# Performance work log

Measured on AMD Instinct MI355X. Metric: run time of the kernel, lower is better.

## Reference

```python
import jax, jax.numpy as jnp
import numpy as np

VOCAB = 32000
D = 512
OUT = 1000
L = 2
H = 8
HD = D // H
MAX_SEQ = 128
ALPHA = 0.5
B, S = 8, 128


def _layernorm(h, g, b, eps=1e-5):
    mu = jnp.mean(h, axis=-1, keepdims=True)
    var = jnp.mean(jnp.square(h - mu), axis=-1, keepdims=True)
    return (h - mu) * jax.lax.rsqrt(var + eps) * g + b


def setup_inputs() -> dict:
    key = jax.random.key(0)
    ks = jax.random.split(key, 20)
    sd = 1.0 / np.sqrt(D)
    inp = {
        "x": jax.random.randint(ks[0], (B, S), 0, VOCAB),
        "steps": 20,
        "tok_emb": jax.random.normal(ks[1], (VOCAB, D), jnp.float32) * 0.02,
        "pos_emb": jax.random.normal(ks[2], (MAX_SEQ, D), jnp.float32) * 0.02,
        # per-layer stacked weights (linear as x @ W + b)
        "Wq": jax.random.normal(ks[3], (L, D, D), jnp.float32) * sd,
        "bq": jnp.zeros((L, D), jnp.float32),
        "Wk": jax.random.normal(ks[4], (L, D, D), jnp.float32) * sd,
        "bk": jnp.zeros((L, D), jnp.float32),
        "Wv": jax.random.normal(ks[5], (L, D, D), jnp.float32) * sd,
        "bv": jnp.zeros((L, D), jnp.float32),
        "Wo": jax.random.normal(ks[6], (L, D, D), jnp.float32) * sd,
        "bo": jnp.zeros((L, D), jnp.float32),
        "W1": jax.random.normal(ks[7], (L, D, 2 * D), jnp.float32) * sd,
        "b1": jnp.zeros((L, 2 * D), jnp.float32),
        "W2": jax.random.normal(ks[8], (L, 2 * D, D), jnp.float32) * (1.0 / np.sqrt(2 * D)),
        "b2": jnp.zeros((L, D), jnp.float32),
        "ln1_g": jnp.ones((L, D), jnp.float32),
        "ln1_b": jnp.zeros((L, D), jnp.float32),
        "ln2_g": jnp.ones((L, D), jnp.float32),
        "ln2_b": jnp.zeros((L, D), jnp.float32),
        "head_w": jax.random.normal(ks[9], (D, OUT), jnp.float32) * sd,
        "head_b": jnp.zeros((OUT,), jnp.float32),
    }
    return inp


def _forward(x, steps, tok_emb, pos_emb, Wq, bq, Wk, bk, Wv, bv, Wo, bo,
             W1, b1, W2, b2, ln1_g, ln1_b, ln2_g, ln2_b, head_w, head_b):
    b, s = x.shape
    x_emb = tok_emb[x] + pos_emb[jnp.arange(s)][None, :, :]  # [B,S,D]
    scale = 1.0 / np.sqrt(HD)

    def step(h, _):
        for i in range(L):
            hn = _layernorm(h, ln1_g[i], ln1_b[i])
            q = (hn @ Wq[i] + bq[i]).reshape(b, s, H, HD)
            k = (hn @ Wk[i] + bk[i]).reshape(b, s, H, HD)
            v = (hn @ Wv[i] + bv[i]).reshape(b, s, H, HD)
            scores = jnp.einsum('bqhd,bkhd->bhqk', q, k) * scale
            attn = jax.nn.softmax(scores, axis=-1)
            o = jnp.einsum('bhqk,bkhd->bqhd', attn, v).reshape(b, s, D)
            h = h + (o @ Wo[i] + bo[i])
            hn2 = _layernorm(h, ln2_g[i], ln2_b[i])
            ffn = jax.nn.relu(hn2 @ W1[i] + b1[i]) @ W2[i] + b2[i]
            h_target = h + ffn + x_emb
            h = h + ALPHA * (jnp.tanh(h_target) - h)  # lerp(h, tanh(t), alpha)
        return h, None

    h0 = jnp.zeros_like(x_emb)
    h, _ = jax.lax.scan(step, h0, None, length=steps)
    return h.mean(axis=1) @ head_w + head_b  # [B, OUT]


def reference(x, steps, tok_emb, pos_emb, Wq, bq, Wk, bk, Wv, bv, Wo, bo,
              W1, b1, W2, b2, ln1_g, ln1_b, ln2_g, ln2_b, head_w, head_b):
    return _forward(x, steps, tok_emb, pos_emb, Wq, bq, Wk, bk, Wv, bv, Wo, bo,
                    W1, b1, W2, b2, ln1_g, ln1_b, ln2_g, ln2_b, head_w, head_b)
```

## Files before the change

### kernel.cpp

```cpp
#include <hip/hip_runtime.h>
#include <hip/hip_bf16.h>
#include <math.h>

#define NTOK 1024
#define DM   512
#define NB   256

typedef unsigned short u16;
typedef __attribute__((ext_vector_type(8))) short short8;
typedef __attribute__((ext_vector_type(4))) float f32x4;
typedef __attribute__((ext_vector_type(2))) float f32x2;
typedef __attribute__((address_space(1))) const void* as1cv;
typedef __attribute__((address_space(3))) void* as3v;

#define VM12 0x0F7C
#define VM16 0x4F70
#define VM8  0x0F78
#define VM0  0x0F70

__device__ inline u16 f2bf(float f) {
  __hip_bfloat16 h = __float2bfloat16(f);
  return *reinterpret_cast<u16*>(&h);
}
__device__ inline float bf2f(u16 b) {
  union { unsigned u; float f; } x; x.u = (unsigned)b << 16; return x.f;
}
__device__ inline void split8(const float* v, short8& hi, short8& lo) {
#pragma unroll
  for (int j = 0; j < 8; j++) {
    u16 h = f2bf(v[j]);
    hi[j] = (short)h;
    lo[j] = (short)f2bf(v[j] - bf2f(h));
  }
}
__device__ __forceinline__ f32x4 MFMA(short8 a, short8 b, f32x4 c) {
  return __builtin_amdgcn_mfma_f32_16x16x32_bf16(a, b, c, 0, 0, 0);
}
__device__ __forceinline__ void atomAddF(float* p, float v) {
  __hip_atomic_fetch_add(p, v, __ATOMIC_RELAXED, __HIP_MEMORY_SCOPE_AGENT);
}

__device__ __forceinline__ f32x2 ldg_cs2(const float* p) {
  f32x2 r;
  asm volatile("global_load_dwordx2 %0, %1, off sc0 sc1" : "=v"(r) : "v"(p) : "memory");
  return r;
}
__device__ __forceinline__ void vmwait0() {
  asm volatile("s_waitcnt vmcnt(0)" ::: "memory");
  __builtin_amdgcn_sched_barrier(0);
}

enum { EP_RESID = 1, EP_TANHLERP = 3 };

struct KArgs {
  const int* x;
  const float* tok; const float* pos;
  const float* W[6];
  const float* bias6[6];
  const float* ln1g; const float* ln1b; const float* ln2g; const float* ln2b;
  const float* hw; const float* hb;
  float* out;
  float* xe; float* h;
  u16* obh; u16* obl;
  u16* ffh; u16* ffl;
  u16* vT;
  float* hm;
  u16* WTh[6]; u16* WTl[6];
  float* ln1sum; float* ln2sum;
  unsigned* bar;
};

#define SMEM_BYTES 49152

__device__ __forceinline__ void bar_arrive(unsigned* ctr, int tid) {
  __syncthreads();
  if (tid == 0)
    __hip_atomic_fetch_add(ctr, 1u, __ATOMIC_RELEASE, __HIP_MEMORY_SCOPE_AGENT);
}
__device__ __forceinline__ void bar_wait(unsigned* ctr, unsigned target, int tid) {
  if (tid == 0) {
    while (__hip_atomic_load(ctr, __ATOMIC_RELAXED, __HIP_MEMORY_SCOPE_AGENT) < target)
      __builtin_amdgcn_s_sleep(2);
    __builtin_amdgcn_fence(__ATOMIC_ACQUIRE, "agent");
  }
  __syncthreads();
}
__device__ __forceinline__ void bar_arrive_fast(unsigned* myslot, unsigned ph, int tid) {
  asm volatile("s_waitcnt vmcnt(0) lgkmcnt(0)" ::: "memory");
  __syncthreads();
  if (tid == 0)
    __hip_atomic_store(myslot, ph, __ATOMIC_RELAXED, __HIP_MEMORY_SCOPE_AGENT);
}
__device__ __forceinline__ void bar_wait_fast(unsigned* slotbase, unsigned ph, int tid) {
  if (tid < 32) {
    while (__hip_atomic_load(slotbase + tid * 16, __ATOMIC_RELAXED,
                             __HIP_MEMORY_SCOPE_AGENT) < ph)
      __builtin_amdgcn_s_sleep(1);
  }
  __syncthreads();
  asm volatile("buffer_inv sc0" ::: "memory");
  asm volatile("s_waitcnt vmcnt(0)" ::: "memory");
}
__global__ void bar_init(unsigned* bar) {
  for (int i = threadIdx.x; i < 8192; i += 256) bar[i] = 0u;
}

__device__ __forceinline__ void dmaW64(const u16* gbase, int K, int k0, u16* lds, int tid) {
  const int wave = tid >> 6, lane = tid & 63;
#pragma unroll
  for (int i = 0; i < 2; i++) {
    const int lc = wave * 128 + i * 64 + lane;
    const int n = lc >> 3, sl = lc & 7;
    const int c = sl ^ (n & 7);
    const u16* g = gbase + (size_t)n * K + k0 + c * 8;
    u16* dst = lds + (size_t)(wave * 128 + i * 64) * 8;
    __builtin_amdgcn_global_load_lds((as1cv)(const void*)g, (as3v)(void*)dst, 16, 0, 0);
  }
}
__device__ __forceinline__ int boff64(int n, int cp) { return n * 64 + ((cp ^ (n & 7)) << 3); }

__device__ __forceinline__ void dmaW32(const u16* gbase, int K, int k0, u16* lds, int tid) {
  const int wave = tid >> 6, lane = tid & 63;
  const int lc = wave * 64 + lane;
  const int p = lc >> 3, s3 = lc & 7;
  const int c3 = s3 ^ (p & 7);
  const int n = p * 2 + (c3 >> 2);
  const int c = c3 & 3;
  const u16* g = gbase + (size_t)n * K + k0 + c * 8;
  u16* dst = lds + (size_t)(wave * 64) * 8;
  __builtin_amdgcn_global_load_lds((as1cv)(const void*)g, (as3v)(void*)dst, 16, 0, 0);
}
__device__ __forceinline__ int boff32(int n, int cq) {
  const int c3 = ((n & 1) << 2) | cq;
  return ((n >> 1) << 6) + ((c3 ^ ((n >> 1) & 7)) << 3);
}

__device__ __forceinline__ void pfBD2(const u16* bh0, const u16* bl0, int K, char* sm, int tid) {
  dmaW64(bh0, K, 0,  (u16*)sm, tid);
  dmaW64(bl0, K, 0,  (u16*)sm + 4096, tid);
  dmaW64(bh0, K, 64, (u16*)(sm + 16384), tid);
  dmaW64(bl0, K, 64, (u16*)(sm + 16384) + 4096, tid);
}
__device__ __forceinline__ void pfA(const KArgs& a, int l, int head, char* sm, int tid) {
  const size_t o = (size_t)l * 512 * 512 + (size_t)head * 64 * 512;
  const u16* wz[6] = { a.WTh[0] + o, a.WTl[0] + o, a.WTh[1] + o,
                       a.WTl[1] + o, a.WTh[2] + o, a.WTl[2] + o };
#pragma unroll
  for (int z = 0; z < 6; z++) dmaW32(wz[z], 512, 0, (u16*)sm + z * 2048, tid);
}

__device__ void phaseA(const KArgs& a, int l, int head, int grp, const float* ln1,
                       const float* hR, u16* obh_g, u16* obl_g, char* sm, int tid)
{
  const int wave = tid >> 6, lane = tid & 63;
  const int q = lane >> 4, r16 = lane & 15;
  const int wm = (wave >> 1) * 32, wn = (wave & 1) * 32;
  const size_t wOff = (size_t)l * 512 * 512;
  const size_t hOff = (size_t)head * 64 * 512;

  const float* lg = a.ln1g + l * 512;
  const float* lb = a.ln1b + l * 512;
  const u16* wz[6] = { a.WTh[0] + wOff + hOff, a.WTl[0] + wOff + hOff,
                       a.WTh[1] + wOff + hOff, a.WTl[1] + wOff + hOff,
                       a.WTh[2] + wOff + hOff, a.WTl[2] + wOff + hOff };
  u16* vT = a.vT + (size_t)(grp * 8 + head) * 64 * 128;
  u16* buf[2] = { (u16*)sm, (u16*)sm + 12288 };

  int RB[4];
#pragma unroll
  for (int fi = 0; fi < 4; fi++) RB[fi] = (fi >> 1) * 64 + wm + (fi & 1) * 16;

  f32x2 st4[4];
#pragma unroll
  for (int fi = 0; fi < 4; fi++) st4[fi] = ldg_cs2(ln1 + (RB[fi] + r16) * 2);
  vmwait0();
  float mu[4], iv[4];
#pragma unroll
  for (int fi = 0; fi < 4; fi++) {
    const float m = st4[fi].x * (1.0f / 512.0f);
    mu[fi] = m;
    iv[fi] = rsqrtf(st4[fi].y * (1.0f / 512.0f) - m * m + 1e-5f);
  }

  f32x4 aq[4][2] = {}, ak[4][2] = {}, av[4][2] = {};

  float4 rA[4][2], rB4[4][2], rg[2], rb[2], rg2[2], rb2[2];
#pragma unroll
  for (int fi = 0; fi < 4; fi++) {
    const float* hp = hR + (size_t)(RB[fi] + r16) * DM + q * 8;
    rA[fi][0] = *(const float4*)hp; rA[fi][1] = *(const float4*)(hp + 4);
  }
  rg[0] = *(const float4*)&lg[q * 8]; rg[1] = *(const float4*)&lg[q * 8 + 4];
  rb[0] = *(const float4*)&lb[q * 8]; rb[1] = *(const float4*)&lb[q * 8 + 4];

  for (int ks = 0; ks < 16; ks++) {
    if (ks + 1 < 16) {
      const int kb = (ks + 1) * 32 + q * 8;
#pragma unroll
      for (int fi = 0; fi < 4; fi++) {
        const float* hp = hR + (size_t)(RB[fi] + r16) * DM + kb;
        rB4[fi][0] = *(const float4*)hp; rB4[fi][1] = *(const float4*)(hp + 4);
      }
      rg2[0] = *(const float4*)&lg[kb]; rg2[1] = *(const float4*)&lg[kb + 4];
      rb2[0] = *(const float4*)&lb[kb]; rb2[1] = *(const float4*)&lb[kb + 4];
      __builtin_amdgcn_s_waitcnt(VM12);
    } else {
      __builtin_amdgcn_s_waitcnt(VM0);
    }
    __builtin_amdgcn_s_barrier();
    if (ks + 1 < 16) {
      u16* nb = buf[(ks + 1) & 1];
#pragma unroll
      for (int z2 = 0; z2 < 6; z2++) dmaW32(wz[z2], 512, (ks + 1) * 32, nb + z2 * 2048, tid);
    }
    const u16* cb = buf[ks & 1];
    short8 ah[4], al[4];
#pragma unroll
    for (int fi = 0; fi < 4; fi++) {
      float v[8] = {
        (rA[fi][0].x - mu[fi]) * iv[fi] * rg[0].x + rb[0].x,
        (rA[fi][0].y - mu[fi]) * iv[fi] * rg[0].y + rb[0].y,
        (rA[fi][0].z - mu[fi]) * iv[fi] * rg[0].z + rb[0].z,
        (rA[fi][0].w - mu[fi]) * iv[fi] * rg[0].w + rb[0].w,
        (rA[fi][1].x - mu[fi]) * iv[fi] * rg[1].x + rb[1].x,
        (rA[fi][1].y - mu[fi]) * iv[fi] * rg[1].y + rb[1].y,
        (rA[fi][1].z - mu[fi]) * iv[fi] * rg[1].z + rb[1].z,
        (rA[fi][1].w - mu[fi]) * iv[fi] * rg[1].w + rb[1].w };
      split8(v, ah[fi], al[fi]);
    }
#pragma unroll
    for (int z = 0; z < 3; z++) {
      f32x4 (*ac)[2] = (z == 0) ? aq : ((z == 1) ? ak : av);
#pragma unroll
      for (int fj = 0; fj < 2; fj++) {
        const int n = wn + fj * 16 + r16;
        const int off = boff32(n, q);
        short8 bh = *(const short8*)&cb[(z * 2) * 2048 + off];
        short8 bl = *(const short8*)&cb[(z * 2 + 1) * 2048 + off];
#pragma unroll
        for (int fi = 0; fi < 4; fi++) {
          ac[fi][fj] = MFMA(ah[fi], bh, ac[fi][fj]);
          ac[fi][fj] = MFMA(ah[fi], bl, ac[fi][fj]);
          ac[fi][fj] = MFMA(al[fi], bh, ac[fi][fj]);
        }
      }
    }
#pragma unroll
    for (int fi = 0; fi < 4; fi++) { rA[fi][0] = rB4[fi][0]; rA[fi][1] = rB4[fi][1]; }
    rg[0] = rg2[0]; rg[1] = rg2[1]; rb[0] = rb2[0]; rb[1] = rb2[1];
  }
  __syncthreads();

  u16 (*Qb)[66] = (u16(*)[66])sm;
  u16 (*Kb)[66] = (u16(*)[66])(sm + 16896);
  {
    const float* bq = a.bias6[0] + l * 512 + head * 64;
    const float* bk = a.bias6[1] + l * 512 + head * 64;
    const float* bv = a.bias6[2] + l * 512 + head * 64;
#pragma unroll
    for (int fi = 0; fi < 4; fi++) {
#pragma unroll
      for (int fj = 0; fj < 2; fj++) {
        const int col = wn + fj * 16 + r16;
        const int row0 = RB[fi] + q * 4;
        const float bqv = bq[col], bkv = bk[col], bvv = bv[col];
#pragma unroll
        for (int i = 0; i < 4; i++) {
          Qb[row0 + i][col] = f2bf(aq[fi][fj][i] + bqv);
          Kb[row0 + i][col] = f2bf(ak[fi][fj][i] + bkv);
          vT[(size_t)col * 128 + row0 + i] = f2bf(av[fi][fj][i] + bvv);
        }
      }
    }
  }
  __syncthreads();

  const int m0 = wave * 32;
  f32x4 sc[2][8] = {};
#pragma unroll
  for (int kk = 0; kk < 2; kk++) {
    short8 aQ[2];
#pragma unroll
    for (int fi = 0; fi < 2; fi++)
      aQ[fi] = *(const short8*)&Qb[m0 + fi * 16 + r16][kk * 32 + q * 8];
#pragma unroll
    for (int nt = 0; nt < 8; nt++) {
      short8 bK = *(const short8*)&Kb[nt * 16 + r16][kk * 32 + q * 8];
#pragma unroll
      for (int fi = 0; fi < 2; fi++) sc[fi][nt] = MFMA(aQ[fi], bK, sc[fi][nt]);
    }
  }
  __syncthreads();

#pragma unroll
  for (int fi = 0; fi < 2; fi++) {
#pragma unroll
    for (int i = 0; i < 4; i++) {
      float mrow = -1e30f;
#pragma unroll
      for (int nt = 0; nt < 8; nt++) {
        float v = sc[fi][nt][i] * 0.125f; sc[fi][nt][i] = v; mrow = fmaxf(mrow, v);
      }
#pragma unroll
      for (int o = 1; o < 16; o <<= 1) mrow = fmaxf(mrow, __shfl_xor(mrow, o, 64));
      float lsum = 0.f;
#pragma unroll
      for (int nt = 0; nt < 8; nt++) {
        float p = __expf(sc[fi][nt][i] - mrow); sc[fi][nt][i] = p; lsum += p;
      }
#pragma unroll
      for (int o = 1; o < 16; o <<= 1) lsum += __shfl_xor(lsum, o, 64);
      const float inv = 1.0f / lsum;
#pragma unroll
      for (int nt = 0; nt < 8; nt++) sc[fi][nt][i] *= inv;
    }
  }
  u16 (*Pb)[132] = (u16(*)[132])sm;
#pragma unroll
  for (int fi = 0; fi < 2; fi++)
#pragma unroll
    for (int nt = 0; nt < 8; nt++)
#pragma unroll
      for (int i = 0; i < 4; i++)
        Pb[m0 + fi * 16 + q * 4 + i][nt * 16 + r16] = f2bf(sc[fi][nt][i]);
  __syncthreads();

  f32x4 oa[2][4] = {};
#pragma unroll
  for (int kt = 0; kt < 4; kt++) {
    short8 aP[2];
#pragma unroll
    for (int fi = 0; fi < 2; fi++)
      aP[fi] = *(const short8*)&Pb[m0 + fi * 16 + r16][kt * 32 + q * 8];
#pragma unroll
    for (int nt = 0; nt < 4; nt++) {
      short8 bV = *(const short8*)(vT + (size_t)(nt * 16 + r16) * 128 + kt * 32 + q * 8);
#pragma unroll
      for (int fi = 0; fi < 2; fi++) oa[fi][nt] = MFMA(aP[fi], bV, oa[fi][nt]);
    }
  }
#pragma unroll
  for (int fi = 0; fi < 2; fi++)
#pragma unroll
    for (int nt = 0; nt < 4; nt++)
#pragma unroll
      for (int i = 0; i < 4; i++) {
        const int row = m0 + fi * 16 + q * 4 + i;
        const int col = head * 64 + nt * 16 + r16;
        float v = oa[fi][nt][i];
        u16 hv = f2bf(v);
        obh_g[(size_t)row * DM + col] = hv;
        obl_g[(size_t)row * DM + col] = f2bf(v - bf2f(hv));
      }
}

template<int EP>
__device__ void tileBD(const u16* Ahi, const u16* Alo, int K,
                       const u16* Whi, const u16* Wlo, const float* bias,
                       int bm, int bn, float* hIO, const float* Xx,
                       float* lnacc, char* sm, int tid)
{
  const int wave = tid >> 6, lane = tid & 63;
  const int q = lane >> 4, r16 = lane & 15;
  const int wm = (wave >> 1) * 16, wn = (wave & 1) * 32;
  const u16* bh0 = Whi + (size_t)bn * K;
  const u16* bl0 = Wlo + (size_t)bn * K;
  f32x4 acc[2] = {};
  const int nk = K >> 6;

  short8 cah[2], cal[2], nh[2], nl[2];
#pragma unroll
  for (int kk = 0; kk < 2; kk++) {
    const size_t ao = (size_t)(bm + wm + r16) * K + kk * 32 + q * 8;
    cah[kk] = *(const short8*)(Ahi + ao);
    cal[kk] = *(const short8*)(Alo + ao);
  }

  for (int ks = 0; ks < nk; ks++) {
    if (ks + 1 < nk) {
#pragma unroll
      for (int kk = 0; kk < 2; kk++) {
        const size_t ao = (size_t)(bm + wm + r16) * K + (ks + 1) * 64 + kk * 32 + q * 8;
        nh[kk] = *(const short8*)(Ahi + ao);
        nl[kk] = *(const short8*)(Alo + ao);
      }
      __builtin_amdgcn_s_waitcnt(VM8);
    } else {
      __builtin_amdgcn_s_waitcnt(VM0);
    }
    __builtin_amdgcn_s_barrier();
    if (ks + 2 < nk) {
      u16* slot = (u16*)(sm + ((ks + 2) % 3) * 16384);
      dmaW64(bh0, K, (ks + 2) * 64, slot, tid);
      dmaW64(bl0, K, (ks + 2) * 64, slot + 4096, tid);
    }
    const u16* Bsh = (const u16*)(sm + (ks % 3) * 16384);
    const u16* Bsl = Bsh + 4096;
#pragma unroll
    for (int kk = 0; kk < 2; kk++) {
#pragma unroll
      for (int fj = 0; fj < 2; fj++) {
        const int n = wn + fj * 16 + r16;
        const int off = boff64(n, kk * 4 + q);
        short8 bh = *(const short8*)&Bsh[off];
        short8 bl = *(const short8*)&Bsl[off];
        acc[fj] = MFMA(cah[kk], bh, acc[fj]);
        acc[fj] = MFMA(cah[kk], bl, acc[fj]);
        acc[fj] = MFMA(cal[kk], bh, acc[fj]);
      }
    }
#pragma unroll
    for (int kk = 0; kk < 2; kk++) { cah[kk] = nh[kk]; cal[kk] = nl[kk]; }
  }

  float outv[2][4];
#pragma unroll
  for (int fj = 0; fj < 2; fj++) {
    const int col = bn + wn + fj * 16 + r16;
    const float bvv = bias[col];
    const int row0 = bm + wm + q * 4;
#pragma unroll
    for (int i = 0; i < 4; i++) {
      const size_t off = (size_t)(row0 + i) * DM + col;
      if (EP == EP_RESID) {
        float hv = hIO[off] + acc[fj][i] + bvv;
        hIO[off] = hv; outv[fj][i] = hv;
      } else {
        float hv = hIO[off];
        float hn = 0.5f * hv + 0.5f * tanhf(hv + acc[fj][i] + bvv + Xx[off]);
        hIO[off] = hn; outv[fj][i] = hn;
      }
    }
  }
#pragma unroll
  for (int i = 0; i < 4; i++) {
    float a0 = outv[0][i], a1 = outv[1][i];
    float s1 = a0 + a1, s2 = a0 * a0 + a1 * a1;
#pragma unroll
    for (int o = 1; o < 16; o <<= 1) { s1 += __shfl_xor(s1, o, 64); s2 += __shfl_xor(s2, o, 64); }
    if (r16 == 0) {
      const int row = bm + wm + q * 4 + i;
      atomAddF(&lnacc[row * 2], s1);
      atomAddF(&lnacc[row * 2 + 1], s2);
    }
  }
}

__device__ void tileC2(const KArgs& a, int l, const float* h_g, const float* lnsrc,
                       u16* ffh_g, u16* ffl_g, int bm, int bn0, char* sm, int tid)
{
  const int wave = tid >> 6, lane = tid & 63;
  const int q = lane >> 4, r16 = lane & 15;
  const int wm = (wave >> 1) * 16, wn = (wave & 1) * 32;
  const size_t fOff = (size_t)l * 512 * 1024;
  const float* lg = a.ln2g + l * 512;
  const float* lb = a.ln2b + l * 512;

  f32x2 stl = ldg_cs2(lnsrc + (bm + wm + r16) * 2);
  vmwait0();
  const float mu = stl.x * (1.0f / 512.0f);
  const float iv = rsqrtf(stl.y * (1.0f / 512.0f) - mu * mu + 1e-5f);

  const u16* whB[2] = { a.WTh[4] + fOff + (size_t)bn0 * 512,
                        a.WTh[4] + fOff + (size_t)(bn0 + 512) * 512 };
  const u16* wlB[2] = { a.WTl[4] + fOff + (size_t)bn0 * 512,
                        a.WTl[4] + fOff + (size_t)(bn0 + 512) * 512 };
  const float* b1 = a.bias6[4] + l * 1024;
  f32x4 acc[2] = {};

  float4 rA[2][2], rB4[2][2], rg[2][2], rb[2][2], rg2[2][2], rb2[2][2];
#pragma unroll
  for (int kk = 0; kk < 2; kk++) {
    const int kb = kk * 32 + q * 8;
    const float* hp = h_g + (size_t)(bm + wm + r16) * DM + kb;
    rA[kk][0] = *(const float4*)hp; rA[kk][1] = *(const float4*)(hp + 4);
    rg[kk][0] = *(const float4*)&lg[kb]; rg[kk][1] = *(const float4*)&lg[kb + 4];
    rb[kk][0] = *(const float4*)&lb[kb]; rb[kk][1] = *(const float4*)&lb[kb + 4];
  }

  for (int s = 0; s < 16; s++) {
    if (s + 1 < 16) {
      const int kb1 = ((s + 1) & 7) * 64;
#pragma unroll
      for (int kk = 0; kk < 2; kk++) {
        const int kb = kb1 + kk * 32 + q * 8;
        const float* hp = h_g + (size_t)(bm + wm + r16) * DM + kb;
        rB4[kk][0] = *(const float4*)hp; rB4[kk][1] = *(const float4*)(hp + 4);
        rg2[kk][0] = *(const float4*)&lg[kb]; rg2[kk][1] = *(const float4*)&lg[kb + 4];
        rb2[kk][0] = *(const float4*)&lb[kb]; rb2[kk][1] = *(const float4*)&lb[kb + 4];
      }
      __builtin_amdgcn_s_waitcnt(VM16);
    } else {
      __builtin_amdgcn_s_waitcnt(VM0);
    }
    __builtin_amdgcn_s_barrier();
    if (s + 2 < 16) {
      const int t2 = (s + 2) >> 3, k2 = ((s + 2) & 7) * 64;
      u16* slot = (u16*)(sm + ((s + 2) % 3) * 16384);
      dmaW64(whB[t2], 512, k2, slot, tid);
      dmaW64(wlB[t2], 512, k2, slot + 4096, tid);
    }
    const u16* Bsh = (const u16*)(sm + (s % 3) * 16384);
    const u16* Bsl = Bsh + 4096;
#pragma unroll
    for (int kk = 0; kk < 2; kk++) {
      short8 ah, al;
      {
        float v[8] = {
          (rA[kk][0].x - mu) * iv * rg[kk][0].x + rb[kk][0].x,
          (rA[kk][0].y - mu) * iv * rg[kk][0].y + rb[kk][0].y,
          (rA[kk][0].z - mu) * iv * rg[kk][0].z + rb[kk][0].z,
          (rA[kk][0].w - mu) * iv * rg[kk][0].w + rb[kk][0].w,
          (rA[kk][1].x - mu) * iv * rg[kk][1].x + rb[kk][1].x,
          (rA[kk][1].y - mu) * iv * rg[kk][1].y + rb[kk][1].y,
          (rA[kk][1].z - mu) * iv * rg[kk][1].z + rb[kk][1].z,
          (rA[kk][1].w - mu) * iv * rg[kk][1].w + rb[kk][1].w };
        split8(v, ah, al);
      }
#pragma unroll
      for (int fj = 0; fj < 2; fj++) {
        const int n = wn + fj * 16 + r16;
        const int off = boff64(n, kk * 4 + q);
        short8 bh = *(const short8*)&Bsh[off];
        short8 bl = *(const short8*)&Bsl[off];
        acc[fj] = MFMA(ah, bh, acc[fj]);
        acc[fj] = MFMA(ah, bl, acc[fj]);
        acc[fj] = MFMA(al, bh, acc[fj]);
      }
    }
    if ((s & 7) == 7) {
      const int t = s >> 3;
#pragma unroll
      for (int fj = 0; fj < 2; fj++) {
        const int col = bn0 + t * 512 + wn + fj * 16 + r16;
        const float bvv = b1[col];
        const int row0 = bm + wm + q * 4;
#pragma unroll
        for (int i = 0; i < 4; i++) {
          const size_t off = (size_t)(row0 + i) * 1024 + col;
          float r = fmaxf(acc[fj][i] + bvv, 0.f);
          u16 hv = f2bf(r);
          ffh_g[off] = hv; ffl_g[off] = f2bf(r - bf2f(hv));
        }
        acc[fj] = (f32x4){0.f, 0.f, 0.f, 0.f};
      }
    }
#pragma unroll
    for (int kk = 0; kk < 2; kk++) {
      rA[kk][0] = rB4[kk][0]; rA[kk][1] = rB4[kk][1];
      rg[kk][0] = rg2[kk][0]; rg[kk][1] = rg2[kk][1];
      rb[kk][0] = rb2[kk][0]; rb[kk][1] = rb2[kk][1];
    }
  }
}

__global__ __launch_bounds__(256, 1) void persist(KArgs a)
{
  __shared__ __align__(16) char smem[SMEM_BYTES];
  const int tid = threadIdx.x;
  const int bid = blockIdx.x;

  unsigned myxcd;
  asm volatile("s_getreg_b32 %0, hwreg(HW_REG_XCC_ID)" : "=s"(myxcd));
  myxcd &= 15u;
  if (tid == 0) a.bar[512 + bid] = myxcd;

  {
    float (*tile)[33] = (float (*)[33])smem;
    const int tx = tid & 31, ty = tid >> 5;
    for (int t = bid; t < 4096; t += NB) {
      int tensor, z, k0, n0, K, N;
      if (t < 2048)      { tensor = t >> 9;  int rem = t & 511;  z = rem >> 8; int r2 = rem & 255;
                           K = 512;  N = 512;  k0 = (r2 >> 4) << 5; n0 = (r2 & 15) << 5; }
      else if (t < 3072) { tensor = 4;       int rem = t - 2048; z = rem >> 9; int r2 = rem & 511;
                           K = 512;  N = 1024; k0 = (r2 >> 5) << 5; n0 = (r2 & 31) << 5; }
      else               { tensor = 5;       int rem = t - 3072; z = rem >> 9; int r2 = rem & 511;
                           K = 1024; N = 512;  k0 = (r2 >> 4) << 5; n0 = (r2 & 15) << 5; }
      const float* src = a.W[tensor]   + (size_t)z * K * N;
      u16* dhi         = a.WTh[tensor] + (size_t)z * K * N;
      u16* dlo         = a.WTl[tensor] + (size_t)z * K * N;
      __syncthreads();
#pragma unroll
      for (int r = 0; r < 4; r++) {
        int k = ty + r * 8;
        tile[k][tx] = src[(size_t)(k0 + k) * N + n0 + tx];
      }
      __syncthreads();
#pragma unroll
      for (int r = 0; r < 4; r++) {
        int n = ty + r * 8;
        float w = tile[tx][n];
        u16 hi = f2bf(w);
        dhi[(size_t)(n0 + n) * K + k0 + tx] = hi;
        dlo[(size_t)(n0 + n) * K + k0 + tx] = f2bf(w - bf2f(hi));
      }
    }
    for (int idx = bid * 256 + tid; idx < NTOK * DM; idx += NB * 256) {
      int t = idx >> 9, d = idx & 511, ss = t & 127;
      a.xe[idx] = a.tok[(size_t)a.x[t] * DM + d] + a.pos[ss * DM + d];
      a.h[idx] = 0.0f;
    }
    const int nstat = (41 + 40) * 8 * 256;
    for (int idx = bid * 256 + tid; idx < nstat; idx += NB * 256)
      a.ln1sum[idx] = 0.0f;
  }
  bar_arrive(a.bar + 256, tid);
  bar_wait(a.bar + 256, NB, tid);

  int grp, gb; bool fast;
  {
    int cnt[8] = {0, 0, 0, 0, 0, 0, 0, 0};
    int rank = 0; bool bad = false;
    for (int j = 0; j < NB; j++) {
      unsigned xj = a.bar[512 + j];
      if (xj > 7u) { bad = true; }
      else {
        cnt[xj]++;
        if (xj == myxcd && j < bid) rank++;
      }
    }
    fast = !bad;
    for (int x2 = 0; x2 < 8; x2++) fast = fast && (cnt[x2] == 32);
    if (fast) { grp = (int)myxcd; gb = rank; }
    else      { grp = bid & 7;    gb = bid >> 3; }
  }

  if (gb < 8) pfA(a, 0, gb, smem, tid);

  unsigned* gctr = a.bar + grp * 32;
  unsigned* slotbase = a.bar + 1024 + grp * 512;
  unsigned* myslot = slotbase + gb * 16;
  unsigned tgt = 0, ph = 0;
  const size_t r512  = (size_t)grp * 128 * 512;
  const size_t r1024 = (size_t)grp * 128 * 1024;
  float* h_g  = a.h  + r512;
  float* xe_g = a.xe + r512;
  u16 *obh_g = a.obh + r512, *obl_g = a.obl + r512;
  u16 *ffh_g = a.ffh + r1024, *ffl_g = a.ffl + r1024;
  const int bn = (gb & 7) * 64, bm = (gb >> 3) * 32;

#define G_ARRIVE() do { ph++; if (fast) bar_arrive_fast(myslot, ph, tid); \
                        else bar_arrive(gctr, tid); } while (0)
#define G_WAIT()   do { if (fast) bar_wait_fast(slotbase, ph, tid); \
                        else { tgt += 32; bar_wait(gctr, tgt, tid); } } while (0)

  for (int it = 0; it < 40; it++) {
    const int l = it & 1;
    const size_t wOff = (size_t)l * 512 * 512;
    const size_t fOff = (size_t)l * 512 * 1024;
    float* ln1it = a.ln1sum + ((size_t)it * 8 + grp) * 256;
    float* ln2it = a.ln2sum + ((size_t)it * 8 + grp) * 256;
    float* ln1nx = a.ln1sum + ((size_t)(it + 1) * 8 + grp) * 256;

    if (gb < 8) phaseA(a, l, gb, grp, ln1it, h_g, obh_g, obl_g, smem, tid);
    G_ARRIVE();
    pfBD2(a.WTh[3] + wOff + (size_t)bn * 512, a.WTl[3] + wOff + (size_t)bn * 512, 512, smem, tid);
    G_WAIT();

    tileBD<EP_RESID>(obh_g, obl_g, 512, a.WTh[3] + wOff, a.WTl[3] + wOff,
                     a.bias6[3] + l * 512, bm, bn, h_g, nullptr, ln2it, smem, tid);
    G_ARRIVE();
    pfBD2(a.WTh[4] + fOff + (size_t)bn * 512, a.WTl[4] + fOff + (size_t)bn * 512, 512, smem, tid);
    G_WAIT();

    tileC2(a, l, h_g, ln2it, ffh_g, ffl_g, bm, bn, smem, tid);
    G_ARRIVE();
    pfBD2(a.WTh[5] + fOff + (size_t)bn * 1024, a.WTl[5] + fOff + (size_t)bn * 1024, 1024, smem, tid);
    G_WAIT();

    tileBD<EP_TANHLERP>(ffh_g, ffl_g, 1024, a.WTh[5] + fOff, a.WTl[5] + fOff,
                        a.bias6[5] + l * 512, bm, bn, h_g, xe_g, ln1nx, smem, tid);
    G_ARRIVE();
    if (it + 1 < 40 && gb < 8) pfA(a, (it + 1) & 1, gb, smem, tid);
    G_WAIT();
  }

  if (gb < 16) {
    const int dim = gb * 32 + (tid >> 3);
    const int sub = tid & 7;
    float sv = 0.f;
    for (int si = sub; si < 128; si += 8) sv += h_g[(size_t)si * DM + dim];
    sv += __shfl_xor(sv, 1, 64); sv += __shfl_xor(sv, 2, 64); sv += __shfl_xor(sv, 4, 64);
    if (sub == 0) a.hm[grp * 512 + dim] = sv * (1.0f / 128.0f);
  }
  G_ARRIVE();
  G_WAIT();

  {
    const int idx = tid >> 2;
    const int n = gb * 63 + idx;
    const int sub = tid & 3;
    if (idx < 63 && n < 1000) {
      const float* hr = a.hm + grp * 512 + sub * 128;
      const float* wr = a.hw + (size_t)(sub * 128) * 1000 + n;
      float sv = 0.f;
      for (int j = 0; j < 128; j++) sv = fmaf(hr[j], wr[(size_t)j * 1000], sv);
      sv += __shfl_xor(sv, 1, 64);
      sv += __shfl_xor(sv, 2, 64);
      if (sub == 0) a.out[grp * 1000 + n] = sv + a.hb[n];
    }
  }
#undef G_ARRIVE
#undef G_WAIT
}

extern "C" void kernel_launch(void* const* d_in, const int* in_sizes, int n_in,
                              void* d_out, int out_size, void* d_ws, size_t ws_size,
                              hipStream_t stream)
{
  (void)in_sizes; (void)n_in; (void)out_size; (void)ws_size;
  KArgs a;
  a.x    = (const int*)d_in[0];
  a.tok  = (const float*)d_in[2];
  a.pos  = (const float*)d_in[3];
  a.W[0] = (const float*)d_in[4];   a.bias6[0] = (const float*)d_in[5];
  a.W[1] = (const float*)d_in[6];   a.bias6[1] = (const float*)d_in[7];
  a.W[2] = (const float*)d_in[8];   a.bias6[2] = (const float*)d_in[9];
  a.W[3] = (const float*)d_in[10];  a.bias6[3] = (const float*)d_in[11];
  a.W[4] = (const float*)d_in[12];  a.bias6[4] = (const float*)d_in[13];
  a.W[5] = (const float*)d_in[14];  a.bias6[5] = (const float*)d_in[15];
  a.ln1g = (const float*)d_in[16];
  a.ln1b = (const float*)d_in[17];
  a.ln2g = (const float*)d_in[18];
  a.ln2b = (const float*)d_in[19];
  a.hw   = (const float*)d_in[20];
  a.hb   = (const float*)d_in[21];
  a.out  = (float*)d_out;

  char* ws = (char*)d_ws;
  const size_t MB = 1ull << 20;
  a.xe   = (float*)(ws + 0 * MB);
  a.h    = (float*)(ws + 2 * MB);
  a.obh  = (u16*)(ws + 4 * MB);
  a.obl  = (u16*)(ws + 5 * MB);
  a.ffh  = (u16*)(ws + 6 * MB);
  a.ffl  = (u16*)(ws + 8 * MB);
  a.hm   = (float*)(ws + 10 * MB);
  a.vT   = (u16*)(ws + 11 * MB);
  a.WTh[0] = (u16*)(ws + 12 * MB);  a.WTl[0] = (u16*)(ws + 13 * MB);
  a.WTh[1] = (u16*)(ws + 14 * MB);  a.WTl[1] = (u16*)(ws + 15 * MB);
  a.WTh[2] = (u16*)(ws + 16 * MB);  a.WTl[2] = (u16*)(ws + 17 * MB);
  a.WTh[3] = (u16*)(ws + 18 * MB);  a.WTl[3] = (u16*)(ws + 19 * MB);
  a.WTh[4] = (u16*)(ws + 20 * MB);  a.WTl[4] = (u16*)(ws + 22 * MB);
  a.WTh[5] = (u16*)(ws + 24 * MB);  a.WTl[5] = (u16*)(ws + 26 * MB);
  a.bar    = (unsigned*)(ws + 28 * MB);
  a.ln1sum = (float*)(ws + 29 * MB);
  a.ln2sum = a.ln1sum + (size_t)41 * 8 * 256;

  bar_init<<<1, 256, 0, stream>>>(a.bar);
  persist<<<NB, 256, 0, stream>>>(a);
}
```

Baseline: 4.080 ms.

## Split attention phase across all blocks per group with an extra grid barrier

The QKV projection and attention phase previously ran on only 8 of 32 blocks per group, one block per head. It now runs on all 32 blocks, each handling a head and a 32-row slice. K and V^T go to global scratch, followed by a group barrier, then a second sub-phase where each block computes softmax attention for its query rows against the full K/V. This spreads the serial attention work across idle blocks, at the cost of one more barrier per layer, global round-trips for K, and weight tiles reloaded by every block.

```diff
diff --git a/kernel.cpp b/kernel.cpp
--- a/kernel.cpp
+++ b/kernel.cpp
@@ -13,9 +13,9 @@
 typedef __attribute__((address_space(1))) const void* as1cv;
 typedef __attribute__((address_space(3))) void* as3v;
 
-#define VM12 0x0F7C
 #define VM16 0x4F70
 #define VM8  0x0F78
+#define VM6  0x0F76
 #define VM0  0x0F70
 
 __device__ inline u16 f2bf(float f) {
@@ -64,6 +64,7 @@
   u16* obh; u16* obl;
   u16* ffh; u16* ffl;
   u16* vT;
+  u16* Kg;
   float* hm;
   u16* WTh[6]; u16* WTl[6];
   float* ln1sum; float* ln2sum;
@@ -149,12 +150,14 @@
   for (int z = 0; z < 6; z++) dmaW32(wz[z], 512, 0, (u16*)sm + z * 2048, tid);
 }
 
-__device__ void phaseA(const KArgs& a, int l, int head, int grp, const float* ln1,
-                       const float* hR, u16* obh_g, u16* obl_g, char* sm, int tid)
+__device__ void phaseA1(const KArgs& a, int l, int head, int rbk, int grp,
+                        const float* ln1, const float* hR,
+                        u16* Kg_gh, u16* vT_gh, char* sm, int tid)
 {
   const int wave = tid >> 6, lane = tid & 63;
   const int q = lane >> 4, r16 = lane & 15;
-  const int wm = (wave >> 1) * 32, wn = (wave & 1) * 32;
+  const int wm = (wave >> 1) * 16, wn = (wave & 1) * 32;
+  const int R0 = rbk * 32;
   const size_t wOff = (size_t)l * 512 * 512;
   const size_t hOff = (size_t)head * 64 * 512;
 
@@ -163,47 +166,30 @@
   const u16* wz[6] = { a.WTh[0] + wOff + hOff, a.WTl[0] + wOff + hOff,
                        a.WTh[1] + wOff + hOff, a.WTl[1] + wOff + hOff,
                        a.WTh[2] + wOff + hOff, a.WTl[2] + wOff + hOff };
-  u16* vT = a.vT + (size_t)(grp * 8 + head) * 64 * 128;
   u16* buf[2] = { (u16*)sm, (u16*)sm + 12288 };
 
-  int RB[4];
-#pragma unroll
-  for (int fi = 0; fi < 4; fi++) RB[fi] = (fi >> 1) * 64 + wm + (fi & 1) * 16;
-
-  f32x2 st4[4];
-#pragma unroll
-  for (int fi = 0; fi < 4; fi++) st4[fi] = ldg_cs2(ln1 + (RB[fi] + r16) * 2);
+  f32x2 st = ldg_cs2(ln1 + (R0 + wm + r16) * 2);
   vmwait0();
-  float mu[4], iv[4];
-#pragma unroll
-  for (int fi = 0; fi < 4; fi++) {
-    const float m = st4[fi].x * (1.0f / 512.0f);
-    mu[fi] = m;
-    iv[fi] = rsqrtf(st4[fi].y * (1.0f / 512.0f) - m * m + 1e-5f);
-  }
-
-  f32x4 aq[4][2] = {}, ak[4][2] = {}, av[4][2] = {};
-
-  float4 rA[4][2], rB4[4][2], rg[2], rb[2], rg2[2], rb2[2];
-#pragma unroll
-  for (int fi = 0; fi < 4; fi++) {
-    const float* hp = hR + (size_t)(RB[fi] + r16) * DM + q * 8;
-    rA[fi][0] = *(const float4*)hp; rA[fi][1] = *(const float4*)(hp + 4);
+  const float mu = st.x * (1.0f / 512.0f);
+  const float iv = rsqrtf(st.y * (1.0f / 512.0f) - mu * mu + 1e-5f);
+
+  f32x4 aq[2] = {}, ak[2] = {}, av[2] = {};
+  float4 rA[2], rB4[2], rg[2], rb_[2], rg2[2], rb2[2];
+  {
+    const float* hp = hR + (size_t)(R0 + wm + r16) * DM + q * 8;
+    rA[0] = *(const float4*)hp; rA[1] = *(const float4*)(hp + 4);
   }
   rg[0] = *(const float4*)&lg[q * 8]; rg[1] = *(const float4*)&lg[q * 8 + 4];
-  rb[0] = *(const float4*)&lb[q * 8]; rb[1] = *(const float4*)&lb[q * 8 + 4];
+  rb_[0] = *(const float4*)&lb[q * 8]; rb_[1] = *(const float4*)&lb[q * 8 + 4];
 
   for (int ks = 0; ks < 16; ks++) {
     if (ks + 1 < 16) {
       const int kb = (ks + 1) * 32 + q * 8;
-#pragma unroll
-      for (int fi = 0; fi < 4; fi++) {
-        const float* hp = hR + (size_t)(RB[fi] + r16) * DM + kb;
-        rB4[fi][0] = *(const float4*)hp; rB4[fi][1] = *(const float4*)(hp + 4);
-      }
+      const float* hp = hR + (size_t)(R0 + wm + r16) * DM + kb;
+      rB4[0] = *(const float4*)hp; rB4[1] = *(const float4*)(hp + 4);
       rg2[0] = *(const float4*)&lg[kb]; rg2[1] = *(const float4*)&lg[kb + 4];
       rb2[0] = *(const float4*)&lb[kb]; rb2[1] = *(const float4*)&lb[kb + 4];
-      __builtin_amdgcn_s_waitcnt(VM12);
+      __builtin_amdgcn_s_waitcnt(VM6);
     } else {
       __builtin_amdgcn_s_waitcnt(VM0);
     }
@@ -214,144 +200,140 @@
       for (int z2 = 0; z2 < 6; z2++) dmaW32(wz[z2], 512, (ks + 1) * 32, nb + z2 * 2048, tid);
     }
     const u16* cb = buf[ks & 1];
-    short8 ah[4], al[4];
-#pragma unroll
-    for (int fi = 0; fi < 4; fi++) {
+    short8 ah, al;
+    {
       float v[8] = {
-        (rA[fi][0].x - mu[fi]) * iv[fi] * rg[0].x + rb[0].x,
-        (rA[fi][0].y - mu[fi]) * iv[fi] * rg[0].y + rb[0].y,
-        (rA[fi][0].z - mu[fi]) * iv[fi] * rg[0].z + rb[0].z,
-        (rA[fi][0].w - mu[fi]) * iv[fi] * rg[0].w + rb[0].w,
-        (rA[fi][1].x - mu[fi]) * iv[fi] * rg[1].x + rb[1].x,
-        (rA[fi][1].y - mu[fi]) * iv[fi] * rg[1].y + rb[1].y,
-        (rA[fi][1].z - mu[fi]) * iv[fi] * rg[1].z + rb[1].z,
-        (rA[fi][1].w - mu[fi]) * iv[fi] * rg[1].w + rb[1].w };
-      split8(v, ah[fi], al[fi]);
+        (rA[0].x - mu) * iv * rg[0].x + rb_[0].x,
+        (rA[0].y - mu) * iv * rg[0].y + rb_[0].y,
+        (rA[0].z - mu) * iv * rg[0].z + rb_[0].z,
+        (rA[0].w - mu) * iv * rg[0].w + rb_[0].w,
+        (rA[1].x - mu) * iv * rg[1].x + rb_[1].x,
+        (rA[1].y - mu) * iv * rg[1].y + rb_[1].y,
+        (rA[1].z - mu) * iv * rg[1].z + rb_[1].z,
+        (rA[1].w - mu) * iv * rg[1].w + rb_[1].w };
+      split8(v, ah, al);
     }
 #pragma unroll
     for (int z = 0; z < 3; z++) {
-      f32x4 (*ac)[2] = (z == 0) ? aq : ((z == 1) ? ak : av);
+      f32x4* ac = (z == 0) ? aq : ((z == 1) ? ak : av);
 #pragma unroll
       for (int fj = 0; fj < 2; fj++) {
         const int n = wn + fj * 16 + r16;
         const int off = boff32(n, q);
         short8 bh = *(const short8*)&cb[(z * 2) * 2048 + off];
         short8 bl = *(const short8*)&cb[(z * 2 + 1) * 2048 + off];
-#pragma unroll
-        for (int fi = 0; fi < 4; fi++) {
-          ac[fi][fj] = MFMA(ah[fi], bh, ac[fi][fj]);
-          ac[fi][fj] = MFMA(ah[fi], bl, ac[fi][fj]);
-          ac[fi][fj] = MFMA(al[fi], bh, ac[fi][fj]);
-        }
-      }
-    }
-#pragma unroll
-    for (int fi = 0; fi < 4; fi++) { rA[fi][0] = rB4[fi][0]; rA[fi][1] = rB4[fi][1]; }
-    rg[0] = rg2[0]; rg[1] = rg2[1]; rb[0] = rb2[0]; rb[1] = rb2[1];
+        ac[fj] = MFMA(ah, bh, ac[fj]);
+        ac[fj] = MFMA(ah, bl, ac[fj]);
+        ac[fj] = MFMA(al, bh, ac[fj]);
+      }
+    }
+    rA[0] = rB4[0]; rA[1] = rB4[1];
+    rg[0] = rg2[0]; rg[1] = rg2[1]; rb_[0] = rb2[0]; rb_[1] = rb2[1];
   }
   __syncthreads();
 
   u16 (*Qb)[66] = (u16(*)[66])sm;
-  u16 (*Kb)[66] = (u16(*)[66])(sm + 16896);
   {
     const float* bq = a.bias6[0] + l * 512 + head * 64;
     const float* bk = a.bias6[1] + l * 512 + head * 64;
     const float* bv = a.bias6[2] + l * 512 + head * 64;
 #pragma unroll
-    for (int fi = 0; fi < 4; fi++) {
-#pragma unroll
-      for (int fj = 0; fj < 2; fj++) {
-        const int col = wn + fj * 16 + r16;
-        const int row0 = RB[fi] + q * 4;
-        const float bqv = bq[col], bkv = bk[col], bvv = bv[col];
-#pragma unroll
-        for (int i = 0; i < 4; i++) {
-          Qb[row0 + i][col] = f2bf(aq[fi][fj][i] + bqv);
-          Kb[row0 + i][col] = f2bf(ak[fi][fj][i] + bkv);
-          vT[(size_t)col * 128 + row0 + i] = f2bf(av[fi][fj][i] + bvv);
-        }
-      }
-    }
+    for (int fj = 0; fj < 2; fj++) {
+      const int col = wn + fj * 16 + r16;
+      const int rl0 = wm + q * 4;
+      const float bqv = bq[col], bkv = bk[col], bvv = bv[col];
+#pragma unroll
+      for (int i = 0; i < 4; i++) {
+        Qb[rl0 + i][col] = f2bf(aq[fj][i] + bqv);
+        Kg_gh[(size_t)(R0 + rl0 + i) * 64 + col] = f2bf(ak[fj][i] + bkv);
+        vT_gh[(size_t)col * 128 + R0 + rl0 + i] = f2bf(av[fj][i] + bvv);
+      }
+    }
+  }
+}
+
+__device__ void phaseA2(const KArgs& a, int head, int rbk,
+                        const u16* Kg_gh, const u16* vT_gh,
+                        u16* obh_g, u16* obl_g, char* sm, int tid)
+{
+  const int wave = tid >> 6, lane = tid & 63;
+  const int q = lane >> 4, r16 = lane & 15;
+  const int R0 = rbk * 32;
+  u16 (*Qb)[66] = (u16(*)[66])sm;
+  u16 (*Kb)[72] = (u16(*)[72])(sm + 4224);
+  u16 (*Pb)[132] = (u16(*)[132])(sm + 22656);
+
+#pragma unroll
+  for (int c = 0; c < 4; c++) {
+    const int lin = (c * 256 + tid) * 8;
+    const int row = lin >> 6, col = lin & 63;
+    *(short8*)&Kb[row][col] = *(const short8*)(Kg_gh + lin);
   }
   __syncthreads();
 
-  const int m0 = wave * 32;
-  f32x4 sc[2][8] = {};
-#pragma unroll
-  for (int kk = 0; kk < 2; kk++) {
-    short8 aQ[2];
-#pragma unroll
-    for (int fi = 0; fi < 2; fi++)
-      aQ[fi] = *(const short8*)&Qb[m0 + fi * 16 + r16][kk * 32 + q * 8];
-#pragma unroll
-    for (int nt = 0; nt < 8; nt++) {
-      short8 bK = *(const short8*)&Kb[nt * 16 + r16][kk * 32 + q * 8];
-#pragma unroll
-      for (int fi = 0; fi < 2; fi++) sc[fi][nt] = MFMA(aQ[fi], bK, sc[fi][nt]);
-    }
-  }
-  __syncthreads();
-
-#pragma unroll
-  for (int fi = 0; fi < 2; fi++) {
+  f32x4 sc[8] = {};
+  const int m0 = (wave & 1) * 16;
+  if (wave < 2) {
+#pragma unroll
+    for (int kk = 0; kk < 2; kk++) {
+      short8 aQ = *(const short8*)&Qb[m0 + r16][kk * 32 + q * 8];
+#pragma unroll
+      for (int nt = 0; nt < 8; nt++) {
+        short8 bK = *(const short8*)&Kb[nt * 16 + r16][kk * 32 + q * 8];
+        sc[nt] = MFMA(aQ, bK, sc[nt]);
+      }
+    }
 #pragma unroll
     for (int i = 0; i < 4; i++) {
       float mrow = -1e30f;
 #pragma unroll
       for (int nt = 0; nt < 8; nt++) {
-        float v = sc[fi][nt][i] * 0.125f; sc[fi][nt][i] = v; mrow = fmaxf(mrow, v);
+        float v = sc[nt][i] * 0.125f; sc[nt][i] = v; mrow = fmaxf(mrow, v);
       }
 #pragma unroll
       for (int o = 1; o < 16; o <<= 1) mrow = fmaxf(mrow, __shfl_xor(mrow, o, 64));
       float lsum = 0.f;
 #pragma unroll
       for (int nt = 0; nt < 8; nt++) {
-        float p = __expf(sc[fi][nt][i] - mrow); sc[fi][nt][i] = p; lsum += p;
+        float p = __expf(sc[nt][i] - mrow); sc[nt][i] = p; lsum += p;
       }
 #pragma unroll
       for (int o = 1; o < 16; o <<= 1) lsum += __shfl_xor(lsum, o, 64);
       const float inv = 1.0f / lsum;
 #pragma unroll
-      for (int nt = 0; nt < 8; nt++) sc[fi][nt][i] *= inv;
-    }
-  }
-  u16 (*Pb)[132] = (u16(*)[132])sm;
-#pragma unroll
-  for (int fi = 0; fi < 2; fi++)
+      for (int nt = 0; nt < 8; nt++) sc[nt][i] *= inv;
+    }
 #pragma unroll
     for (int nt = 0; nt < 8; nt++)
 #pragma unroll
       for (int i = 0; i < 4; i++)
-        Pb[m0 + fi * 16 + q * 4 + i][nt * 16 + r16] = f2bf(sc[fi][nt][i]);
+        Pb[m0 + q * 4 + i][nt * 16 + r16] = f2bf(sc[nt][i]);
+  }
   __syncthreads();
 
-  f32x4 oa[2][4] = {};
-#pragma unroll
-  for (int kt = 0; kt < 4; kt++) {
-    short8 aP[2];
-#pragma unroll
-    for (int fi = 0; fi < 2; fi++)
-      aP[fi] = *(const short8*)&Pb[m0 + fi * 16 + r16][kt * 32 + q * 8];
-#pragma unroll
-    for (int nt = 0; nt < 4; nt++) {
-      short8 bV = *(const short8*)(vT + (size_t)(nt * 16 + r16) * 128 + kt * 32 + q * 8);
-#pragma unroll
-      for (int fi = 0; fi < 2; fi++) oa[fi][nt] = MFMA(aP[fi], bV, oa[fi][nt]);
-    }
-  }
-#pragma unroll
-  for (int fi = 0; fi < 2; fi++)
+  if (wave < 2) {
+    f32x4 oa[4] = {};
+#pragma unroll
+    for (int kt = 0; kt < 4; kt++) {
+      short8 aP = *(const short8*)&Pb[m0 + r16][kt * 32 + q * 8];
+#pragma unroll
+      for (int nt = 0; nt < 4; nt++) {
+        short8 bV = *(const short8*)(vT_gh + (size_t)(nt * 16 + r16) * 128 + kt * 32 + q * 8);
+        oa[nt] = MFMA(aP, bV, oa[nt]);
+      }
+    }
 #pragma unroll
     for (int nt = 0; nt < 4; nt++)
 #pragma unroll
       for (int i = 0; i < 4; i++) {
-        const int row = m0 + fi * 16 + q * 4 + i;
+        const int row = R0 + m0 + q * 4 + i;
         const int col = head * 64 + nt * 16 + r16;
-        float v = oa[fi][nt][i];
+        float v = oa[nt][i];
         u16 hv = f2bf(v);
         obh_g[(size_t)row * DM + col] = hv;
         obl_g[(size_t)row * DM + col] = f2bf(v - bf2f(hv));
       }
+  }
 }
 
 template<int EP>
@@ -625,7 +607,8 @@
     else      { grp = bid & 7;    gb = bid >> 3; }
   }
 
-  if (gb < 8) pfA(a, 0, gb, smem, tid);
+  const int head = gb & 7, rbk = gb >> 3;
+  pfA(a, 0, head, smem, tid);
 
   unsigned* gctr = a.bar + grp * 32;
   unsigned* slotbase = a.bar + 1024 + grp * 512;
@@ -637,6 +620,8 @@
   float* xe_g = a.xe + r512;
   u16 *obh_g = a.obh + r512, *obl_g = a.obl + r512;
   u16 *ffh_g = a.ffh + r1024, *ffl_g = a.ffl + r1024;
+  u16* Kg_gh = a.Kg + (size_t)(grp * 8 + head) * 128 * 64;
+  u16* vT_gh = a.vT + (size_t)(grp * 8 + head) * 64 * 128;
   const int bn = (gb & 7) * 64, bm = (gb >> 3) * 32;
 
 #define G_ARRIVE() do { ph++; if (fast) bar_arrive_fast(myslot, ph, tid); \
@@ -652,7 +637,11 @@
     float* ln2it = a.ln2sum + ((size_t)it * 8 + grp) * 256;
     float* ln1nx = a.ln1sum + ((size_t)(it + 1) * 8 + grp) * 256;
 
-    if (gb < 8) phaseA(a, l, gb, grp, ln1it, h_g, obh_g, obl_g, smem, tid);
+    phaseA1(a, l, head, rbk, grp, ln1it, h_g, Kg_gh, vT_gh, smem, tid);
+    G_ARRIVE();
+    G_WAIT();
+
+    phaseA2(a, head, rbk, Kg_gh, vT_gh, obh_g, obl_g, smem, tid);
     G_ARRIVE();
     pfBD2(a.WTh[3] + wOff + (size_t)bn * 512, a.WTl[3] + wOff + (size_t)bn * 512, 512, smem, tid);
     G_WAIT();
@@ -671,7 +660,7 @@
     tileBD<EP_TANHLERP>(ffh_g, ffl_g, 1024, a.WTh[5] + fOff, a.WTl[5] + fOff,
                         a.bias6[5] + l * 512, bm, bn, h_g, xe_g, ln1nx, smem, tid);
     G_ARRIVE();
-    if (it + 1 < 40 && gb < 8) pfA(a, (it + 1) & 1, gb, smem, tid);
+    if (it + 1 < 40) pfA(a, (it + 1) & 1, head, smem, tid);
     G_WAIT();
   }
 
@@ -746,6 +735,7 @@
   a.bar    = (unsigned*)(ws + 28 * MB);
   a.ln1sum = (float*)(ws + 29 * MB);
   a.ln2sum = a.ln1sum + (size_t)41 * 8 * 256;
+  a.Kg     = (u16*)(ws + 30 * MB);
 
   bar_init<<<1, 256, 0, stream>>>(a.bar);
   persist<<<NB, 256, 0, stream>>>(a);
```

Result: faster. 3.292 ms (-19.3%).
